# Optimization experiments

Measured on AMD Instinct MI355X. Metric: run time of the kernel, lower is better.

Reference implementation:

```python
import jax, jax.numpy as jnp
import numpy as np

B, N, DIM = 2, 512, 128
HEADS, DH = 4, 64
INNER = HEADS * DH            # 256
POS_HID = 64
MULT = 4                      # attn_mlp_hidden_mult
K = 16                        # num_neighbors


def setup_inputs() -> dict:
    key = jax.random.key(0)
    ks = jax.random.split(key, 10)
    w = lambda k, shape: jax.random.normal(k, shape, jnp.float32) * 0.02
    return {
        "x": jax.random.normal(ks[0], (B, N, DIM), jnp.float32),
        "pos": jax.random.normal(ks[1], (B, N, 3), jnp.float32),
        "mask": jnp.ones((B, N), dtype=bool),
        "w_qkv": w(ks[2], (DIM, 3 * INNER)),
        "w_out": w(ks[3], (INNER, DIM)),
        "b_out": jnp.zeros((DIM,), jnp.float32),
        "w_pos1": w(ks[4], (3, POS_HID)),
        "b_pos1": jnp.zeros((POS_HID,), jnp.float32),
        "w_pos2": w(ks[5], (POS_HID, INNER)),
        "b_pos2": jnp.zeros((INNER,), jnp.float32),
        # grouped 1x1 convs == per-head linear layers
        "w_attn1": w(ks[6], (HEADS, DH, MULT * DH)),
        "b_attn1": jnp.zeros((HEADS, MULT * DH), jnp.float32),
        "w_attn2": w(ks[7], (HEADS, MULT * DH, DH)),
        "b_attn2": jnp.zeros((HEADS, DH), jnp.float32),
    }


def reference(x, pos, mask, w_qkv, w_out, b_out, w_pos1, b_pos1, w_pos2, b_pos2,
              w_attn1, b_attn1, w_attn2, b_attn2):
    b, n, _ = x.shape
    h, d = HEADS, DH

    qkv = x @ w_qkv                                   # [b, n, 3*inner]
    q, k, v = jnp.split(qkv, 3, axis=-1)
    to_heads = lambda t: t.reshape(b, n, h, d).transpose(0, 2, 1, 3)  # b h n d
    q, k, v = map(to_heads, (q, k, v))

    # dense pairwise relative positions + pos MLP  [b, n, n, inner]
    rel_pos = pos[:, :, None, :] - pos[:, None, :, :]            # [b, n, n, 3]
    rpe = jax.nn.relu(rel_pos @ w_pos1 + b_pos1) @ w_pos2 + b_pos2

    # masked topk over pairwise distance (smallest K)
    rel_dist = jnp.linalg.norm(rel_pos, axis=-1)                 # [b, n, n]
    mask2 = mask[:, :, None] & mask[:, None, :]                  # [b, n, n]
    fmax = jnp.finfo(rel_dist.dtype).max
    rel_dist = jnp.where(mask2, rel_dist, fmax)
    _, idx = jax.lax.top_k(-rel_dist, K)                         # [b, n, K]

    # neighbor gathers (equivalent to torch batched_index_select over j)
    gather_hd = jax.vmap(lambda t, i: t[:, i, :])                # [h,n,d],[n,K] -> [h,n,K,d]
    k_nb = gather_hd(k, idx)                                     # [b, h, n, K, d]
    v_nb = gather_hd(v, idx)
    row = jnp.arange(n)[:, None]
    rpe_nb = jax.vmap(lambda r, i: r[row, i])(rpe, idx)          # [b, n, K, inner]
    rpe_nb = rpe_nb.reshape(b, n, K, h, d).transpose(0, 3, 1, 2, 4)  # [b,h,n,K,d]
    mask_nb = jax.vmap(lambda m, i: m[row, i])(mask2, idx)       # [b, n, K]

    # qk_rel gathered implicitly: (q_i - k_j)[j=idx] == q_i - k_nb
    attn_in = q[:, :, :, None, :] - k_nb + rpe_nb                # [b, h, n, K, d]

    # grouped 1x1 conv MLP == per-head MLP on last dim
    hid = jax.nn.relu(jnp.einsum('bhikd,hde->bhike', attn_in, w_attn1)
                      + b_attn1[None, :, None, None, :])
    sim = (jnp.einsum('bhike,hed->bhikd', hid, w_attn2)
           + b_attn2[None, :, None, None, :])                    # [b, h, n, K, d]

    sim = jnp.where(mask_nb[:, None, :, :, None], sim, -fmax)
    # torch: sim is [b, (h d), i, j]; softmax(dim=-2) is over i -> axis 2 here
    attn = jax.nn.softmax(sim, axis=2)

    v_full = v_nb + rpe_nb                                       # [b, h, n, K, d]
    agg = jnp.sum(attn * v_full, axis=3)                         # [b, h, n, d]
    agg = agg.transpose(0, 2, 1, 3).reshape(b, n, h * d)         # [b, n, inner]
    return agg @ w_out + b_out
```

## Files before the change

### kernel.cpp

```cpp
#include <hip/hip_runtime.h>

#define B_ 2
#define N_ 512
#define DIM_ 128
#define HEADS_ 4
#define DH_ 64
#define INNER_ 256
#define PH_ 64
#define HID2_ 256
#define KNB_ 16

typedef unsigned long long u64;
typedef unsigned int u32;
typedef unsigned short u16;
typedef __attribute__((ext_vector_type(8))) short bf16x8;
typedef __attribute__((ext_vector_type(8))) unsigned short us8;
typedef __attribute__((ext_vector_type(4))) float f32x4;

__device__ __forceinline__ float bf2f(u16 u) {
    union { float f; u32 u; } c; c.u = ((u32)u) << 16; return c.f;
}
__device__ __forceinline__ u16 f2bf(float f) {
    union { float f; u32 u; } c; c.f = f;
    u32 u = c.u;
    return (u16)((u + 0x7fffu + ((u >> 16) & 1u)) >> 16);
}
__device__ __forceinline__ u32 pack2(float lo, float hi) {
    return ((u32)f2bf(hi) << 16) | (u32)f2bf(lo);
}

__global__ __launch_bounds__(256) void k_front(
        const float* __restrict__ x, const float* __restrict__ pos, const float* __restrict__ w_qkv,
        const float* __restrict__ w_a1, const float* __restrict__ w_a2, const float* __restrict__ w_p2,
        u16* __restrict__ w1T, u16* __restrict__ w2T, u16* __restrict__ w2pT,
        u16* __restrict__ qb, u16* __restrict__ kb, float* __restrict__ v,
        int* __restrict__ idx) {
    int blk = blockIdx.x;
    if (blk < 576) {
        int t = blk * 256 + threadIdx.x;
        if (t < 65536) {
            int h = t >> 14, e = (t >> 6) & 255, d = t & 63;
            w1T[t] = f2bf(w_a1[((h * 64 + d) << 8) + e]);
        } else if (t < 131072) {
            int t2 = t - 65536; int h = t2 >> 14, c = (t2 >> 8) & 63, e = t2 & 255;
            w2T[t2] = f2bf(w_a2[(((h << 8) + e) << 6) + c]);
        } else {
            int t3 = t - 131072; int c = t3 >> 6, e = t3 & 63;
            w2pT[t3] = f2bf(w_p2[(e << 8) + c]);
        }
    } else if (blk < 832) {
        int bu = blk - 576;
        int b = bu >> 7;
        int n0 = (bu & 127) * 4;
        int t = threadIdx.x;
        __shared__ float xs[4][128];
        #pragma unroll
        for (int p = 0; p < 2; ++p) {
            int e = p * 256 + t;
            xs[e >> 7][e & 127] = x[((size_t)(b * N_ + n0) + (e >> 7)) * DIM_ + (e & 127)];
        }
        __syncthreads();
        float acc[3][4];
        #pragma unroll
        for (int cc = 0; cc < 3; ++cc)
            #pragma unroll
            for (int r = 0; r < 4; ++r) acc[cc][r] = 0.f;
        for (int c4 = 0; c4 < 32; ++c4) {
            float wv[3][4];
            #pragma unroll
            for (int dd = 0; dd < 4; ++dd)
                #pragma unroll
                for (int cc = 0; cc < 3; ++cc)
                    wv[cc][dd] = w_qkv[(size_t)(c4 * 4 + dd) * (3 * INNER_) + cc * INNER_ + t];
            #pragma unroll
            for (int r = 0; r < 4; ++r) {
                float4 xv = *(const float4*)&xs[r][c4 * 4];
                #pragma unroll
                for (int cc = 0; cc < 3; ++cc)
                    acc[cc][r] += xv.x * wv[cc][0] + xv.y * wv[cc][1] + xv.z * wv[cc][2] + xv.w * wv[cc][3];
            }
        }
        int h = t >> 6, d = t & 63;
        #pragma unroll
        for (int r = 0; r < 4; ++r) {
            size_t o = (((size_t)(b * HEADS_ + h)) * N_ + n0 + r) * DH_ + d;
            qb[o] = f2bf(acc[0][r]);
            kb[o] = f2bf(acc[1][r]);
            v[o]  = acc[2][r];
        }
    } else {
        int wave = (blk - 832) * 4 + (threadIdx.x >> 6);
        int lane = threadIdx.x & 63;
        int b = wave >> 9;
        float px = pos[(size_t)wave * 3 + 0];
        float py = pos[(size_t)wave * 3 + 1];
        float pz = pos[(size_t)wave * 3 + 2];
        u64 keys[8];
        #pragma unroll
        for (int s = 0; s < 8; ++s) {
            int j = s * 64 + lane;
            float dx = __fsub_rn(px, pos[(size_t)(b * N_ + j) * 3 + 0]);
            float dy = __fsub_rn(py, pos[(size_t)(b * N_ + j) * 3 + 1]);
            float dz = __fsub_rn(pz, pos[(size_t)(b * N_ + j) * 3 + 2]);
            float s2 = __fadd_rn(__fadd_rn(__fmul_rn(dx, dx), __fmul_rn(dy, dy)), __fmul_rn(dz, dz));
            float dist = __fsqrt_rn(s2);
            keys[s] = ((u64)__float_as_uint(dist) << 32) | (unsigned)j;
        }
        for (int r = 0; r < KNB_; ++r) {
            u64 m = keys[0];
            #pragma unroll
            for (int s = 1; s < 8; ++s) m = (keys[s] < m) ? keys[s] : m;
            #pragma unroll
            for (int off = 32; off >= 1; off >>= 1) {
                u64 o = __shfl_xor(m, off);
                m = (o < m) ? o : m;
            }
            if (lane == 0) idx[(size_t)wave * KNB_ + r] = (int)(m & 0xffffffffu);
            #pragma unroll
            for (int s = 0; s < 8; ++s) if (keys[s] == m) keys[s] = ~0ull;
        }
    }
}

__global__ __launch_bounds__(256) void k_attn(
        const u16* __restrict__ qb, const u16* __restrict__ kb, const float* __restrict__ v,
        const int* __restrict__ idx,
        const float* __restrict__ pos, const float* __restrict__ w_p1, const float* __restrict__ b_p1,
        const float* __restrict__ b_p2, const u16* __restrict__ w2pT,
        const u16* __restrict__ w1T, const u16* __restrict__ w2T,
        const float* __restrict__ b_a1, const float* __restrict__ b_a2,
        u16* __restrict__ sim, u16* __restrict__ vf) {
    __shared__ u16 w1s[256 * 72];
    __shared__ u16 w2s[64 * 264];
    __shared__ u16 wps[64 * 72];
    __shared__ u16 HID[4][2][16 * 264];
    int t = threadIdx.x;
    int wv = t >> 6, l = t & 63, lr = l & 15, g = l >> 4;
    int blk = blockIdx.x;
    int bh = blk >> 6, grp = blk & 63;
    int b = bh >> 2, h = bh & 3;
    int i0 = grp * 8 + wv * 2;

    int jn[2];
    float rx[2], ry[2], rz[2];
    us8 qv[2][2], kv[2][2];
    float vvr[2][2][8];
    #pragma unroll
    for (int ii = 0; ii < 2; ++ii) {
        int i = i0 + ii;
        int bi = (b << 9) + i;
        int j = idx[(bi << 4) + lr];
        jn[ii] = j;
        int bj = (b << 9) + j;
        rx[ii] = pos[(size_t)bi * 3 + 0] - pos[(size_t)bj * 3 + 0];
        ry[ii] = pos[(size_t)bi * 3 + 1] - pos[(size_t)bj * 3 + 1];
        rz[ii] = pos[(size_t)bi * 3 + 2] - pos[(size_t)bj * 3 + 2];
        #pragma unroll
        for (int s = 0; s < 2; ++s) {
            qv[ii][s] = *(const us8*)&qb[(size_t)(bh * N_ + i) * 64 + s * 32 + g * 8];
            kv[ii][s] = *(const us8*)&kb[(size_t)(bh * N_ + j) * 64 + s * 32 + g * 8];
            *(float4*)&vvr[ii][s][0] = *(const float4*)&v[(size_t)(bh * N_ + j) * 64 + s * 32 + g * 8];
            *(float4*)&vvr[ii][s][4] = *(const float4*)&v[(size_t)(bh * N_ + j) * 64 + s * 32 + g * 8 + 4];
        }
    }

    {
        const u16* wg = w1T + ((size_t)h << 14);
        for (int c = t; c < 2048; c += 256) {
            int r = c >> 3, c8 = (c & 7) << 3;
            *(bf16x8*)&w1s[r * 72 + c8] = *(const bf16x8*)&wg[(r << 6) + c8];
        }
    }
    {
        const u16* wg = w2T + ((size_t)h << 14);
        for (int c = t; c < 2048; c += 256) {
            int r = c >> 5, c8 = (c & 31) << 3;
            *(bf16x8*)&w2s[r * 264 + c8] = *(const bf16x8*)&wg[(r << 8) + c8];
        }
    }
    {
        const u16* wg = w2pT + ((size_t)h << 12);
        for (int c = t; c < 512; c += 256) {
            int r = c >> 3, c8 = (c & 7) << 3;
            *(bf16x8*)&wps[r * 72 + c8] = *(const bf16x8*)&wg[(r << 6) + c8];
        }
    }
    __syncthreads();

    bf16x8 hidp[2][2];
    #pragma unroll
    for (int ii = 0; ii < 2; ++ii) {
        #pragma unroll
        for (int s = 0; s < 2; ++s) {
            u16 tmp[8];
            #pragma unroll
            for (int jj = 0; jj < 8; ++jj) {
                int e = s * 32 + g * 8 + jj;
                float hh = b_p1[e] + rx[ii] * w_p1[e] + ry[ii] * w_p1[PH_ + e] + rz[ii] * w_p1[2 * PH_ + e];
                tmp[jj] = f2bf(fmaxf(hh, 0.f));
            }
            hidp[ii][s] = *(bf16x8*)tmp;
        }
    }

    #pragma unroll
    for (int ct = 0; ct < 4; ++ct) {
        f32x4 C0 = {0.f, 0.f, 0.f, 0.f}, C1 = {0.f, 0.f, 0.f, 0.f};
        #pragma unroll
        for (int s = 0; s < 2; ++s) {
            bf16x8 A = *(const bf16x8*)&wps[(ct * 16 + lr) * 72 + s * 32 + g * 8];
            C0 = __builtin_amdgcn_mfma_f32_16x16x32_bf16(A, hidp[0][s], C0, 0, 0, 0);
            C1 = __builtin_amdgcn_mfma_f32_16x16x32_bf16(A, hidp[1][s], C1, 0, 0, 0);
        }
        float4 bias = *(const float4*)&b_p2[h * 64 + ct * 16 + g * 4];
        uint2 o0, o1;
        o0.x = pack2(C0[0] + bias.x, C0[1] + bias.y);
        o0.y = pack2(C0[2] + bias.z, C0[3] + bias.w);
        o1.x = pack2(C1[0] + bias.x, C1[1] + bias.y);
        o1.y = pack2(C1[2] + bias.z, C1[3] + bias.w);
        *(uint2*)&HID[wv][0][lr * 264 + ct * 16 + g * 4] = o0;
        *(uint2*)&HID[wv][1][lr * 264 + ct * 16 + g * 4] = o1;
    }

    bf16x8 ain[2][2];
    #pragma unroll
    for (int ii = 0; ii < 2; ++ii) {
        int i = i0 + ii;
        #pragma unroll
        for (int s = 0; s < 2; ++s) {
            bf16x8 rp = *(const bf16x8*)&HID[wv][ii][lr * 264 + s * 32 + g * 8];
            us8 rpu = *(const us8*)&rp;
            u16 ta[8], tv[8];
            #pragma unroll
            for (int jj = 0; jj < 8; ++jj) {
                float rpf = bf2f(rpu[jj]);
                ta[jj] = f2bf(bf2f(qv[ii][s][jj]) - bf2f(kv[ii][s][jj]) + rpf);
                tv[jj] = f2bf(vvr[ii][s][jj] + rpf);
            }
            ain[ii][s] = *(bf16x8*)ta;
            *(bf16x8*)&vf[(size_t)(((bh * N_ + i) << 4) + lr) * 64 + s * 32 + g * 8] = *(bf16x8*)tv;
        }
    }

    for (int et = 0; et < 16; ++et) {
        f32x4 C0 = {0.f, 0.f, 0.f, 0.f}, C1 = {0.f, 0.f, 0.f, 0.f};
        #pragma unroll
        for (int s = 0; s < 2; ++s) {
            bf16x8 A = *(const bf16x8*)&w1s[(et * 16 + lr) * 72 + s * 32 + g * 8];
            C0 = __builtin_amdgcn_mfma_f32_16x16x32_bf16(A, ain[0][s], C0, 0, 0, 0);
            C1 = __builtin_amdgcn_mfma_f32_16x16x32_bf16(A, ain[1][s], C1, 0, 0, 0);
        }
        float4 bias = *(const float4*)&b_a1[h * 256 + et * 16 + g * 4];
        uint2 p0, p1;
        p0.x = pack2(fmaxf(C0[0] + bias.x, 0.f), fmaxf(C0[1] + bias.y, 0.f));
        p0.y = pack2(fmaxf(C0[2] + bias.z, 0.f), fmaxf(C0[3] + bias.w, 0.f));
        p1.x = pack2(fmaxf(C1[0] + bias.x, 0.f), fmaxf(C1[1] + bias.y, 0.f));
        p1.y = pack2(fmaxf(C1[2] + bias.z, 0.f), fmaxf(C1[3] + bias.w, 0.f));
        *(uint2*)&HID[wv][0][lr * 264 + et * 16 + g * 4] = p0;
        *(uint2*)&HID[wv][1][lr * 264 + et * 16 + g * 4] = p1;
    }

    f32x4 C2[2][4];
    #pragma unroll
    for (int ii = 0; ii < 2; ++ii)
        #pragma unroll
        for (int ct = 0; ct < 4; ++ct) C2[ii][ct] = (f32x4){0.f, 0.f, 0.f, 0.f};
    for (int s = 0; s < 8; ++s) {
        bf16x8 B0 = *(const bf16x8*)&HID[wv][0][lr * 264 + s * 32 + g * 8];
        bf16x8 B1 = *(const bf16x8*)&HID[wv][1][lr * 264 + s * 32 + g * 8];
        #pragma unroll
        for (int ct = 0; ct < 4; ++ct) {
            bf16x8 A = *(const bf16x8*)&w2s[(ct * 16 + lr) * 264 + s * 32 + g * 8];
            C2[0][ct] = __builtin_amdgcn_mfma_f32_16x16x32_bf16(A, B0, C2[0][ct], 0, 0, 0);
            C2[1][ct] = __builtin_amdgcn_mfma_f32_16x16x32_bf16(A, B1, C2[1][ct], 0, 0, 0);
        }
    }
    #pragma unroll
    for (int ii = 0; ii < 2; ++ii) {
        int i = i0 + ii;
        #pragma unroll
        for (int ct = 0; ct < 4; ++ct) {
            float4 bias = *(const float4*)&b_a2[h * 64 + ct * 16 + g * 4];
            uint2 o;
            o.x = pack2(C2[ii][ct][0] + bias.x, C2[ii][ct][1] + bias.y);
            o.y = pack2(C2[ii][ct][2] + bias.z, C2[ii][ct][3] + bias.w);
            *(uint2*)&sim[(size_t)(((bh * N_ + i) << 4) + lr) * 64 + ct * 16 + g * 4] = o;
        }
    }
}

__global__ __launch_bounds__(256) void k_stats(const u16* __restrict__ sim, float* __restrict__ P) {
    int blk = blockIdx.x;
    int c = blk & 3, ks = (blk >> 2) & 15, bh = blk >> 6;
    int d = threadIdx.x & 63, sub = threadIdx.x >> 6;
    __shared__ float red[4][64];
    size_t base = ((size_t)(bh * N_) * 16 + ks) * 64 + d;
    int n0 = c * 128 + sub * 32;
    float s = 0.f;
    for (int n = n0; n < n0 + 32; ++n) s += __expf(bf2f(sim[base + (size_t)n * 1024]));
    red[sub][d] = s;
    __syncthreads();
    if (sub == 0) P[blk * 64 + d] = red[0][d] + red[1][d] + red[2][d] + red[3][d];
}

__global__ void k_rsum(const float* __restrict__ P, float* __restrict__ R) {
    int col = blockIdx.x * 256 + threadIdx.x;
    int hi = col >> 6, d = col & 63;
    float s = P[hi * 256 + d] + P[hi * 256 + 64 + d] + P[hi * 256 + 128 + d] + P[hi * 256 + 192 + d];
    R[col] = 1.f / s;
}

__global__ __launch_bounds__(256) void k_agg_out(
        const u16* __restrict__ sim, const u16* __restrict__ vf, const float* __restrict__ R,
        const float* __restrict__ w, const float* __restrict__ bo, float* __restrict__ out) {
    int blk = blockIdx.x;
    int b = blk >> 8;
    int i0 = (blk & 255) * 2;
    int t = threadIdx.x;
    __shared__ float ag[2][260];
    {
        int h = t >> 6, d = t & 63;
        int bh = b * HEADS_ + h;
        float Rk[16];
        #pragma unroll
        for (int ks = 0; ks < 16; ++ks) Rk[ks] = R[((bh << 4) + ks) * 64 + d];
        #pragma unroll
        for (int r = 0; r < 2; ++r) {
            size_t base = (size_t)((bh * N_ + i0 + r) << 4) * 64 + d;
            float acc = 0.f;
            #pragma unroll
            for (int ks = 0; ks < 16; ++ks) {
                float p = __expf(bf2f(sim[base + (size_t)ks * 64])) * Rk[ks];
                acc += p * bf2f(vf[base + (size_t)ks * 64]);
            }
            ag[r][h * 64 + d] = acc;
        }
    }
    __syncthreads();
    int c = t & 127, rg = t >> 7;
    float acc = bo[c];
    for (int k4 = 0; k4 < 64; ++k4) {
        float4 a4 = *(const float4*)&ag[rg][k4 * 4];
        acc += a4.x * w[(size_t)(k4 * 4 + 0) * DIM_ + c] + a4.y * w[(size_t)(k4 * 4 + 1) * DIM_ + c]
             + a4.z * w[(size_t)(k4 * 4 + 2) * DIM_ + c] + a4.w * w[(size_t)(k4 * 4 + 3) * DIM_ + c];
    }
    out[(size_t)((b << 9) + i0 + rg) * DIM_ + c] = acc;
}

extern "C" void kernel_launch(void* const* d_in, const int* in_sizes, int n_in,
                              void* d_out, int out_size, void* d_ws, size_t ws_size,
                              hipStream_t stream) {
    const float* x      = (const float*)d_in[0];
    const float* pos    = (const float*)d_in[1];
    const float* w_qkv  = (const float*)d_in[3];
    const float* w_out  = (const float*)d_in[4];
    const float* b_out  = (const float*)d_in[5];
    const float* w_pos1 = (const float*)d_in[6];
    const float* b_pos1 = (const float*)d_in[7];
    const float* w_pos2 = (const float*)d_in[8];
    const float* b_pos2 = (const float*)d_in[9];
    const float* w_a1   = (const float*)d_in[10];
    const float* b_a1   = (const float*)d_in[11];
    const float* w_a2   = (const float*)d_in[12];
    const float* b_a2   = (const float*)d_in[13];
    float* out = (float*)d_out;

    char* W = (char*)d_ws;
    u16*  qb   = (u16*)W;            W += 524288;
    u16*  kb   = (u16*)W;            W += 524288;
    float* v   = (float*)W;          W += 1048576;
    int*  idx  = (int*)W;            W += 65536;
    u16*  sim  = (u16*)W;            W += 8388608;
    u16*  vf   = (u16*)W;            W += 8388608;
    float* P   = (float*)W;          W += 131072;
    float* R   = (float*)W;          W += 32768;
    u16*  w1T  = (u16*)W;            W += 131072;
    u16*  w2T  = (u16*)W;            W += 131072;
    u16*  w2pT = (u16*)W;            W += 32768;

    k_front<<<1088, 256, 0, stream>>>(x, pos, w_qkv, w_a1, w_a2, w_pos2,
                                      w1T, w2T, w2pT, qb, kb, v, idx);
    k_attn<<<512, 256, 0, stream>>>(qb, kb, v, idx, pos, w_pos1, b_pos1, b_pos2, w2pT,
                                    w1T, w2T, b_a1, b_a2, sim, vf);
    k_stats<<<512, 256, 0, stream>>>(sim, P);
    k_rsum<<<32, 256, 0, stream>>>(P, R);
    k_agg_out<<<512, 256, 0, stream>>>(sim, vf, R, w_out, b_out, out);
}
```

Measured before the change: 70.48 us.

## Enlarge per-block work in QKV, attention MLP and output kernels to reuse weights

The QKV projection now computes 16 rows per block instead of 4, so each loaded weight is reused across more rows. The attention kernel uses 512-thread blocks covering 16 query points, which halves the number of per-block weight loads into shared memory. The hidden MLP is split into two halves so a smaller hidden buffer fits eight waves in shared memory. The output projection processes 4 rows per block and reuses each w_out load for two rows. The cost is fewer blocks in the grid, more registers per thread, and lower occupancy in the QKV and attention stages.

```diff
diff --git a/kernel.cpp b/kernel.cpp
--- a/kernel.cpp
+++ b/kernel.cpp
@@ -48,23 +48,23 @@
             int t3 = t - 131072; int c = t3 >> 6, e = t3 & 63;
             w2pT[t3] = f2bf(w_p2[(e << 8) + c]);
         }
-    } else if (blk < 832) {
+    } else if (blk < 640) {
         int bu = blk - 576;
-        int b = bu >> 7;
-        int n0 = (bu & 127) * 4;
+        int b = bu >> 5;
+        int n0 = (bu & 31) * 16;
         int t = threadIdx.x;
-        __shared__ float xs[4][128];
-        #pragma unroll
-        for (int p = 0; p < 2; ++p) {
+        __shared__ float xs[16][128];
+        #pragma unroll
+        for (int p = 0; p < 8; ++p) {
             int e = p * 256 + t;
             xs[e >> 7][e & 127] = x[((size_t)(b * N_ + n0) + (e >> 7)) * DIM_ + (e & 127)];
         }
         __syncthreads();
-        float acc[3][4];
+        float acc[3][16];
         #pragma unroll
         for (int cc = 0; cc < 3; ++cc)
             #pragma unroll
-            for (int r = 0; r < 4; ++r) acc[cc][r] = 0.f;
+            for (int r = 0; r < 16; ++r) acc[cc][r] = 0.f;
         for (int c4 = 0; c4 < 32; ++c4) {
             float wv[3][4];
             #pragma unroll
@@ -73,7 +73,7 @@
                 for (int cc = 0; cc < 3; ++cc)
                     wv[cc][dd] = w_qkv[(size_t)(c4 * 4 + dd) * (3 * INNER_) + cc * INNER_ + t];
             #pragma unroll
-            for (int r = 0; r < 4; ++r) {
+            for (int r = 0; r < 16; ++r) {
                 float4 xv = *(const float4*)&xs[r][c4 * 4];
                 #pragma unroll
                 for (int cc = 0; cc < 3; ++cc)
@@ -82,14 +82,14 @@
         }
         int h = t >> 6, d = t & 63;
         #pragma unroll
-        for (int r = 0; r < 4; ++r) {
+        for (int r = 0; r < 16; ++r) {
             size_t o = (((size_t)(b * HEADS_ + h)) * N_ + n0 + r) * DH_ + d;
             qb[o] = f2bf(acc[0][r]);
             kb[o] = f2bf(acc[1][r]);
             v[o]  = acc[2][r];
         }
     } else {
-        int wave = (blk - 832) * 4 + (threadIdx.x >> 6);
+        int wave = (blk - 640) * 4 + (threadIdx.x >> 6);
         int lane = threadIdx.x & 63;
         int b = wave >> 9;
         float px = pos[(size_t)wave * 3 + 0];
@@ -122,7 +122,7 @@
     }
 }
 
-__global__ __launch_bounds__(256) void k_attn(
+__global__ __launch_bounds__(512) void k_attn(
         const u16* __restrict__ qb, const u16* __restrict__ kb, const float* __restrict__ v,
         const int* __restrict__ idx,
         const float* __restrict__ pos, const float* __restrict__ w_p1, const float* __restrict__ b_p1,
@@ -133,18 +133,18 @@
     __shared__ u16 w1s[256 * 72];
     __shared__ u16 w2s[64 * 264];
     __shared__ u16 wps[64 * 72];
-    __shared__ u16 HID[4][2][16 * 264];
+    __shared__ u16 HID[8][2][16 * 136];
     int t = threadIdx.x;
     int wv = t >> 6, l = t & 63, lr = l & 15, g = l >> 4;
     int blk = blockIdx.x;
-    int bh = blk >> 6, grp = blk & 63;
+    int bh = blk >> 5, grp = blk & 31;
     int b = bh >> 2, h = bh & 3;
-    int i0 = grp * 8 + wv * 2;
-
-    int jn[2];
+    int i0 = grp * 16 + wv * 2;
+
     float rx[2], ry[2], rz[2];
     us8 qv[2][2], kv[2][2];
     float vvr[2][2][8];
+    int jn[2];
     #pragma unroll
     for (int ii = 0; ii < 2; ++ii) {
         int i = i0 + ii;
@@ -166,24 +166,26 @@
 
     {
         const u16* wg = w1T + ((size_t)h << 14);
-        for (int c = t; c < 2048; c += 256) {
+        #pragma unroll
+        for (int p = 0; p < 4; ++p) {
+            int c = p * 512 + t;
             int r = c >> 3, c8 = (c & 7) << 3;
             *(bf16x8*)&w1s[r * 72 + c8] = *(const bf16x8*)&wg[(r << 6) + c8];
         }
     }
     {
         const u16* wg = w2T + ((size_t)h << 14);
-        for (int c = t; c < 2048; c += 256) {
+        #pragma unroll
+        for (int p = 0; p < 4; ++p) {
+            int c = p * 512 + t;
             int r = c >> 5, c8 = (c & 31) << 3;
             *(bf16x8*)&w2s[r * 264 + c8] = *(const bf16x8*)&wg[(r << 8) + c8];
         }
     }
     {
         const u16* wg = w2pT + ((size_t)h << 12);
-        for (int c = t; c < 512; c += 256) {
-            int r = c >> 3, c8 = (c & 7) << 3;
-            *(bf16x8*)&wps[r * 72 + c8] = *(const bf16x8*)&wg[(r << 6) + c8];
-        }
+        int r = t >> 3, c8 = (t & 7) << 3;
+        *(bf16x8*)&wps[r * 72 + c8] = *(const bf16x8*)&wg[(r << 6) + c8];
     }
     __syncthreads();
 
@@ -218,8 +220,8 @@
         o0.y = pack2(C0[2] + bias.z, C0[3] + bias.w);
         o1.x = pack2(C1[0] + bias.x, C1[1] + bias.y);
         o1.y = pack2(C1[2] + bias.z, C1[3] + bias.w);
-        *(uint2*)&HID[wv][0][lr * 264 + ct * 16 + g * 4] = o0;
-        *(uint2*)&HID[wv][1][lr * 264 + ct * 16 + g * 4] = o1;
+        *(uint2*)&HID[wv][0][lr * 136 + ct * 16 + g * 4] = o0;
+        *(uint2*)&HID[wv][1][lr * 136 + ct * 16 + g * 4] = o1;
     }
 
     bf16x8 ain[2][2];
@@ -228,7 +230,7 @@
         int i = i0 + ii;
         #pragma unroll
         for (int s = 0; s < 2; ++s) {
-            bf16x8 rp = *(const bf16x8*)&HID[wv][ii][lr * 264 + s * 32 + g * 8];
+            bf16x8 rp = *(const bf16x8*)&HID[wv][ii][lr * 136 + s * 32 + g * 8];
             us8 rpu = *(const us8*)&rp;
             u16 ta[8], tv[8];
             #pragma unroll
@@ -242,37 +244,43 @@
         }
     }
 
-    for (int et = 0; et < 16; ++et) {
-        f32x4 C0 = {0.f, 0.f, 0.f, 0.f}, C1 = {0.f, 0.f, 0.f, 0.f};
-        #pragma unroll
-        for (int s = 0; s < 2; ++s) {
-            bf16x8 A = *(const bf16x8*)&w1s[(et * 16 + lr) * 72 + s * 32 + g * 8];
-            C0 = __builtin_amdgcn_mfma_f32_16x16x32_bf16(A, ain[0][s], C0, 0, 0, 0);
-            C1 = __builtin_amdgcn_mfma_f32_16x16x32_bf16(A, ain[1][s], C1, 0, 0, 0);
-        }
-        float4 bias = *(const float4*)&b_a1[h * 256 + et * 16 + g * 4];
-        uint2 p0, p1;
-        p0.x = pack2(fmaxf(C0[0] + bias.x, 0.f), fmaxf(C0[1] + bias.y, 0.f));
-        p0.y = pack2(fmaxf(C0[2] + bias.z, 0.f), fmaxf(C0[3] + bias.w, 0.f));
-        p1.x = pack2(fmaxf(C1[0] + bias.x, 0.f), fmaxf(C1[1] + bias.y, 0.f));
-        p1.y = pack2(fmaxf(C1[2] + bias.z, 0.f), fmaxf(C1[3] + bias.w, 0.f));
-        *(uint2*)&HID[wv][0][lr * 264 + et * 16 + g * 4] = p0;
-        *(uint2*)&HID[wv][1][lr * 264 + et * 16 + g * 4] = p1;
-    }
-
     f32x4 C2[2][4];
     #pragma unroll
     for (int ii = 0; ii < 2; ++ii)
         #pragma unroll
         for (int ct = 0; ct < 4; ++ct) C2[ii][ct] = (f32x4){0.f, 0.f, 0.f, 0.f};
-    for (int s = 0; s < 8; ++s) {
-        bf16x8 B0 = *(const bf16x8*)&HID[wv][0][lr * 264 + s * 32 + g * 8];
-        bf16x8 B1 = *(const bf16x8*)&HID[wv][1][lr * 264 + s * 32 + g * 8];
-        #pragma unroll
-        for (int ct = 0; ct < 4; ++ct) {
-            bf16x8 A = *(const bf16x8*)&w2s[(ct * 16 + lr) * 264 + s * 32 + g * 8];
-            C2[0][ct] = __builtin_amdgcn_mfma_f32_16x16x32_bf16(A, B0, C2[0][ct], 0, 0, 0);
-            C2[1][ct] = __builtin_amdgcn_mfma_f32_16x16x32_bf16(A, B1, C2[1][ct], 0, 0, 0);
+    #pragma unroll
+    for (int half = 0; half < 2; ++half) {
+        #pragma unroll
+        for (int etL = 0; etL < 8; ++etL) {
+            int et = half * 8 + etL;
+            f32x4 C0 = {0.f, 0.f, 0.f, 0.f}, C1 = {0.f, 0.f, 0.f, 0.f};
+            #pragma unroll
+            for (int s = 0; s < 2; ++s) {
+                bf16x8 A = *(const bf16x8*)&w1s[(et * 16 + lr) * 72 + s * 32 + g * 8];
+                C0 = __builtin_amdgcn_mfma_f32_16x16x32_bf16(A, ain[0][s], C0, 0, 0, 0);
+                C1 = __builtin_amdgcn_mfma_f32_16x16x32_bf16(A, ain[1][s], C1, 0, 0, 0);
+            }
+            float4 bias = *(const float4*)&b_a1[h * 256 + et * 16 + g * 4];
+            uint2 p0, p1;
+            p0.x = pack2(fmaxf(C0[0] + bias.x, 0.f), fmaxf(C0[1] + bias.y, 0.f));
+            p0.y = pack2(fmaxf(C0[2] + bias.z, 0.f), fmaxf(C0[3] + bias.w, 0.f));
+            p1.x = pack2(fmaxf(C1[0] + bias.x, 0.f), fmaxf(C1[1] + bias.y, 0.f));
+            p1.y = pack2(fmaxf(C1[2] + bias.z, 0.f), fmaxf(C1[3] + bias.w, 0.f));
+            *(uint2*)&HID[wv][0][lr * 136 + etL * 16 + g * 4] = p0;
+            *(uint2*)&HID[wv][1][lr * 136 + etL * 16 + g * 4] = p1;
+        }
+        #pragma unroll
+        for (int sL = 0; sL < 4; ++sL) {
+            int s = half * 4 + sL;
+            bf16x8 B0 = *(const bf16x8*)&HID[wv][0][lr * 136 + sL * 32 + g * 8];
+            bf16x8 B1 = *(const bf16x8*)&HID[wv][1][lr * 136 + sL * 32 + g * 8];
+            #pragma unroll
+            for (int ct = 0; ct < 4; ++ct) {
+                bf16x8 A = *(const bf16x8*)&w2s[(ct * 16 + lr) * 264 + s * 32 + g * 8];
+                C2[0][ct] = __builtin_amdgcn_mfma_f32_16x16x32_bf16(A, B0, C2[0][ct], 0, 0, 0);
+                C2[1][ct] = __builtin_amdgcn_mfma_f32_16x16x32_bf16(A, B1, C2[1][ct], 0, 0, 0);
+            }
         }
     }
     #pragma unroll
@@ -314,10 +322,10 @@
         const u16* __restrict__ sim, const u16* __restrict__ vf, const float* __restrict__ R,
         const float* __restrict__ w, const float* __restrict__ bo, float* __restrict__ out) {
     int blk = blockIdx.x;
-    int b = blk >> 8;
-    int i0 = (blk & 255) * 2;
+    int b = blk >> 7;
+    int i0 = (blk & 127) * 4;
     int t = threadIdx.x;
-    __shared__ float ag[2][260];
+    __shared__ float ag[4][260];
     {
         int h = t >> 6, d = t & 63;
         int bh = b * HEADS_ + h;
@@ -325,7 +333,7 @@
         #pragma unroll
         for (int ks = 0; ks < 16; ++ks) Rk[ks] = R[((bh << 4) + ks) * 64 + d];
         #pragma unroll
-        for (int r = 0; r < 2; ++r) {
+        for (int r = 0; r < 4; ++r) {
             size_t base = (size_t)((bh * N_ + i0 + r) << 4) * 64 + d;
             float acc = 0.f;
             #pragma unroll
@@ -338,13 +346,21 @@
     }
     __syncthreads();
     int c = t & 127, rg = t >> 7;
-    float acc = bo[c];
+    float acc[2];
+    acc[0] = bo[c]; acc[1] = bo[c];
     for (int k4 = 0; k4 < 64; ++k4) {
-        float4 a4 = *(const float4*)&ag[rg][k4 * 4];
-        acc += a4.x * w[(size_t)(k4 * 4 + 0) * DIM_ + c] + a4.y * w[(size_t)(k4 * 4 + 1) * DIM_ + c]
-             + a4.z * w[(size_t)(k4 * 4 + 2) * DIM_ + c] + a4.w * w[(size_t)(k4 * 4 + 3) * DIM_ + c];
-    }
-    out[(size_t)((b << 9) + i0 + rg) * DIM_ + c] = acc;
+        float wv[4];
+        #pragma unroll
+        for (int kk = 0; kk < 4; ++kk) wv[kk] = w[(size_t)(k4 * 4 + kk) * DIM_ + c];
+        #pragma unroll
+        for (int rr = 0; rr < 2; ++rr) {
+            float4 a4 = *(const float4*)&ag[rr * 2 + rg][k4 * 4];
+            acc[rr] += a4.x * wv[0] + a4.y * wv[1] + a4.z * wv[2] + a4.w * wv[3];
+        }
+    }
+    #pragma unroll
+    for (int rr = 0; rr < 2; ++rr)
+        out[(size_t)((b << 9) + i0 + rr * 2 + rg) * DIM_ + c] = acc[rr];
 }
 
 extern "C" void kernel_launch(void* const* d_in, const int* in_sizes, int n_in,
@@ -378,11 +394,11 @@
     u16*  w2T  = (u16*)W;            W += 131072;
     u16*  w2pT = (u16*)W;            W += 32768;
 
-    k_front<<<1088, 256, 0, stream>>>(x, pos, w_qkv, w_a1, w_a2, w_pos2,
-                                      w1T, w2T, w2pT, qb, kb, v, idx);
-    k_attn<<<512, 256, 0, stream>>>(qb, kb, v, idx, pos, w_pos1, b_pos1, b_pos2, w2pT,
+    k_front<<<896, 256, 0, stream>>>(x, pos, w_qkv, w_a1, w_a2, w_pos2,
+                                     w1T, w2T, w2pT, qb, kb, v, idx);
+    k_attn<<<256, 512, 0, stream>>>(qb, kb, v, idx, pos, w_pos1, b_pos1, b_pos2, w2pT,
                                     w1T, w2T, b_a1, b_a2, sim, vf);
     k_stats<<<512, 256, 0, stream>>>(sim, P);
     k_rsum<<<32, 256, 0, stream>>>(P, R);
-    k_agg_out<<<512, 256, 0, stream>>>(sim, vf, R, w_out, b_out, out);
-}
+    k_agg_out<<<256, 256, 0, stream>>>(sim, vf, R, w_out, b_out, out);
+}
```

Result: slower. 78.68 us (+11.6%).
